# Kernel tuning notes

Hardware: AMD Instinct MI355X
Metric: run time of the kernel (lower is better)

The kernel has to match this reference:

```python
import jax, jax.numpy as jnp
import numpy as np

EPS = 1e-5
NUM_HEADS = 8
KEY_DEPTH = 128   # base_filters * key_expansion
VAL_DEPTH = 256   # base_filters * value_expansion
C_IN = 256


def conv1x1(x, w):
    # x: [N, Cin, L], w: [Cout, Cin] (1x1 conv, no bias)
    return jnp.einsum('oc,ncl->nol', w, x)


def group_norm1(x, w, b, eps=EPS):
    # torch GroupNorm(1, C) on [N, C, L]: normalize over (C, L) per sample,
    # per-channel affine.
    mu = jnp.mean(x, axis=(1, 2), keepdims=True)
    var = jnp.var(x, axis=(1, 2), keepdims=True)
    xn = (x - mu) * jax.lax.rsqrt(var + eps)
    return xn * w[None, :, None] + b[None, :, None]


def layer_norm_last2(x, eps=EPS):
    # freshly-constructed nn.LayerNorm([A, B]): weight=1, bias=0 -> pure norm
    mu = jnp.mean(x, axis=(-2, -1), keepdims=True)
    var = jnp.var(x, axis=(-2, -1), keepdims=True)
    return (x - mu) * jax.lax.rsqrt(var + eps)


def gelu(x):
    return jax.nn.gelu(x, approximate=False)  # torch F.gelu default (erf)


def setup_inputs() -> dict:
    key = jax.random.key(0)
    ks = jax.random.split(key, 16)
    N, L = 8, 1024
    qkv_out = 2 * KEY_DEPTH + VAL_DEPTH  # 512

    def w(k, shape, std=0.02):
        return jax.random.normal(k, shape, jnp.float32) * std

    def gw(k, c):
        return 1.0 + 0.1 * jax.random.normal(k, (c,), jnp.float32)

    return {
        'f': jax.random.normal(ks[0], (N, C_IN, L), jnp.float32),
        'w_z': w(ks[1], (C_IN, C_IN), np.sqrt(2.0 / C_IN)),
        'gz_w': gw(ks[2], C_IN), 'gz_b': w(ks[3], (C_IN,)),
        'w_qkv': w(ks[4], (qkv_out, C_IN), C_IN ** -0.5),
        'gq_w': gw(ks[5], qkv_out), 'gq_b': w(ks[6], (qkv_out,)),
        'w_out': w(ks[7], (C_IN, VAL_DEPTH), np.sqrt(2.0 / VAL_DEPTH)),
        'go_w': gw(ks[8], C_IN), 'go_b': w(ks[9], (C_IN,)),
        'w_ffn1': w(ks[10], (2 * C_IN, C_IN), np.sqrt(2.0 / C_IN)),
        'g1_w': gw(ks[11], 2 * C_IN), 'g1_b': w(ks[12], (2 * C_IN,)),
        'w_ffn2': w(ks[13], (C_IN, 2 * C_IN), np.sqrt(1.0 / C_IN)),
        'g2_w': gw(ks[14], C_IN), 'g2_b': w(ks[15], (C_IN,)),
    }


def reference(f, w_z, gz_w, gz_b, w_qkv, gq_w, gq_b, w_out, go_w, go_b,
              w_ffn1, g1_w, g1_b, w_ffn2, g2_w, g2_b):
    N, C, L = f.shape
    H = NUM_HEADS

    z = gelu(group_norm1(conv1x1(gelu(f), w_z), gz_w, gz_b))
    qkv = group_norm1(conv1x1(z, w_qkv), gq_w, gq_b)
    q, k, v = jnp.split(qkv, [KEY_DEPTH, 2 * KEY_DEPTH], axis=1)
    q = q.reshape(N, H, KEY_DEPTH // H, L)
    k = k.reshape(N, H, KEY_DEPTH // H, L)
    v = v.reshape(N, H, VAL_DEPTH // H, L)

    # [N, H, L, L] similarity, no scaling, then LayerNorm over full LxL map
    logits = jnp.einsum('nhcl,nhcm->nhlm', q, k)
    logits = layer_norm_last2(logits)

    # scatter-mask: diagonal -> -inf for every head
    eye = jnp.eye(L, dtype=bool)[None, None]  # [1,1,L,L]
    logits = jnp.where(eye, -jnp.inf, logits)

    attn = jax.nn.softmax(logits.astype(jnp.float32), axis=-1)
    attn = jnp.where(jnp.isnan(attn), 0.0, attn)

    out = jnp.einsum('nhlm,nhdm->nhdl', attn, v).reshape(N, VAL_DEPTH, L)
    out = gelu(layer_norm_last2(out))  # LayerNorm([C_v, L]), fresh params

    out = group_norm1(conv1x1(out, w_out), go_w, go_b)
    f = gelu(f + out)

    h = gelu(group_norm1(conv1x1(f, w_ffn1), g1_w, g1_b))
    h = group_norm1(conv1x1(h, w_ffn2), g2_w, g2_b)
    return gelu(f + h)
```

## Files before the change

### kernel.cpp

```cpp
#include <hip/hip_runtime.h>

#define LSEQ 1024

typedef __attribute__((ext_vector_type(8))) short bf16x8;
typedef __attribute__((ext_vector_type(4))) float f32x4;

__device__ __forceinline__ float gelu_f(float x){
    return 0.5f*x*(1.0f+erff(x*0.7071067811865476f));
}

__device__ __forceinline__ unsigned f2bf1(float x){
    unsigned u = __float_as_uint(x);
    return (u + 0x7fffu + ((u>>16)&1u)) >> 16;
}
__device__ __forceinline__ unsigned packbf(float lo, float hi){
    return f2bf1(lo) | (f2bf1(hi)<<16);
}

__global__ __launch_bounds__(256) void pack_weights(
    const float* __restrict__ w0, const float* __restrict__ w1,
    const float* __restrict__ w2, const float* __restrict__ w3,
    const float* __restrict__ w4, unsigned short* __restrict__ dst)
{
    int idx4 = blockIdx.x*256 + threadIdx.x;
    const float* src; int off4;
    if(idx4 < 16384){ src=w0; off4=idx4; }
    else if(idx4 < 49152){ src=w1; off4=idx4-16384; }
    else if(idx4 < 65536){ src=w2; off4=idx4-49152; }
    else if(idx4 < 98304){ src=w3; off4=idx4-65536; }
    else { src=w4; off4=idx4-98304; }
    float4 v = ((const float4*)src)[off4];
    uint2 p; p.x = packbf(v.x,v.y); p.y = packbf(v.z,v.w);
    ((uint2*)dst)[idx4] = p;
}

__global__ __launch_bounds__(256,2) void xform_bf16(
    const float* __restrict__ src, const float* __restrict__ res,
    const float* __restrict__ stats,
    const float* __restrict__ gw, const float* __restrict__ gb,
    float cnt_inv, int C, unsigned short* __restrict__ dst)
{
    __shared__ float T[64][68];
    int n = blockIdx.z;
    int ltile = blockIdx.x*64, ctile = blockIdx.y*64;
    int tid = threadIdx.x;

    float mu=0.f, istd=1.f;
    if(stats){
        float s1 = stats[2*n], s2 = stats[2*n+1];
        mu = s1*cnt_inv;
        istd = rsqrtf(s2*cnt_inv - mu*mu + 1e-5f);
    }
    const float* s = src + (size_t)n*C*LSEQ;
    const float* r = res ? res + (size_t)n*C*LSEQ : nullptr;

    int cl = tid>>4, l4 = (tid&15)*4;
    #pragma unroll
    for(int p=0;p<4;p++){
        int c_loc = p*16 + cl;
        int c = ctile + c_loc;
        float w_ = 1.f, b_ = 0.f;
        if(stats){ w_ = istd; b_ = -mu*istd; }
        if(gw){ b_ = gb[c] + b_*gw[c]; w_ *= gw[c]; }
        float4 v = *(const float4*)&s[(size_t)c*LSEQ + ltile + l4];
        float4 t;
        t.x = v.x*w_+b_; t.y = v.y*w_+b_; t.z = v.z*w_+b_; t.w = v.w*w_+b_;
        if(r){
            float4 rv = *(const float4*)&r[(size_t)c*LSEQ + ltile + l4];
            t.x += rv.x; t.y += rv.y; t.z += rv.z; t.w += rv.w;
        }
        t.x = gelu_f(t.x); t.y = gelu_f(t.y); t.z = gelu_f(t.z); t.w = gelu_f(t.w);
        *(float4*)&T[c_loc][l4] = t;
    }
    __syncthreads();

    int l_loc = tid>>2, cg = (tid&3)*16;
    uint4 o0, o1;
    o0.x = packbf(T[cg+0][l_loc],  T[cg+1][l_loc]);
    o0.y = packbf(T[cg+2][l_loc],  T[cg+3][l_loc]);
    o0.z = packbf(T[cg+4][l_loc],  T[cg+5][l_loc]);
    o0.w = packbf(T[cg+6][l_loc],  T[cg+7][l_loc]);
    o1.x = packbf(T[cg+8][l_loc],  T[cg+9][l_loc]);
    o1.y = packbf(T[cg+10][l_loc], T[cg+11][l_loc]);
    o1.z = packbf(T[cg+12][l_loc], T[cg+13][l_loc]);
    o1.w = packbf(T[cg+14][l_loc], T[cg+15][l_loc]);
    unsigned short* d = dst + (size_t)n*LSEQ*C + (size_t)(ltile+l_loc)*C + ctile + cg;
    *(uint4*)d = o0;
    *(uint4*)(d+8) = o1;
}

__global__ __launch_bounds__(256,2) void gemm_bf16(
    const unsigned short* __restrict__ Abf,
    const unsigned short* __restrict__ Bbf,
    float* __restrict__ C,
    int M, int K,
    float* __restrict__ out_stats)
{
    __shared__ short As[64*40];
    __shared__ short Bs[64*40];

    int tid = threadIdx.x;
    int n = blockIdx.z, n0 = blockIdx.x*64, m0 = blockIdx.y*64;
    int wave = tid>>6, lane = tid&63;
    int col = lane&15, quad = lane>>4;
    int sr = tid>>2, sk = (tid&3)*8;

    const unsigned short* apt = Abf + (size_t)(m0+sr)*K + sk;
    const unsigned short* bpt = Bbf + ((size_t)n*LSEQ + n0+sr)*K + sk;

    f32x4 acc[4];
    #pragma unroll
    for(int t=0;t<4;t++) acc[t] = (f32x4){0.f,0.f,0.f,0.f};

    uint4 a = *(const uint4*)apt;
    uint4 b = *(const uint4*)bpt;

    for(int k0=0; k0<K; k0+=32){
        __syncthreads();
        *(uint4*)&As[sr*40 + sk] = a;
        *(uint4*)&Bs[sr*40 + sk] = b;
        __syncthreads();
        if(k0+32 < K){
            a = *(const uint4*)(apt + k0+32);
            b = *(const uint4*)(bpt + k0+32);
        }
        bf16x8 af = *(bf16x8*)&As[(wave*16+col)*40 + quad*8];
        #pragma unroll
        for(int t=0;t<4;t++){
            bf16x8 bf = *(bf16x8*)&Bs[(t*16+col)*40 + quad*8];
            acc[t] = __builtin_amdgcn_mfma_f32_16x16x32_bf16(af, bf, acc[t], 0,0,0);
        }
    }

    __syncthreads();
    size_t cbase = (size_t)n*M*LSEQ;
    float lsum=0.f, lsq=0.f;
    #pragma unroll
    for(int t=0;t<4;t++){
        #pragma unroll
        for(int r2=0;r2<4;r2++){
            int m = m0 + wave*16 + quad*4 + r2;
            int l = n0 + t*16 + col;
            float v = acc[t][r2];
            C[cbase + (size_t)m*LSEQ + l] = v;
            lsum += v; lsq += v*v;
        }
    }
    float* scr = (float*)As;
    scr[tid] = lsum; scr[256+tid] = lsq;
    __syncthreads();
    for(int s=128;s>0;s>>=1){
        if(tid<s){ scr[tid]+=scr[tid+s]; scr[256+tid]+=scr[256+tid+s]; }
        __syncthreads();
    }
    if(tid==0){
        atomicAdd(&out_stats[2*n],   scr[0]);
        atomicAdd(&out_stats[2*n+1], scr[256]);
    }
}

__global__ __launch_bounds__(256,2) void head_cov(
    const float* __restrict__ qkv,
    const float* __restrict__ s_qkv,
    const float* __restrict__ gq_w, const float* __restrict__ gq_b,
    float* __restrict__ covq, float* __restrict__ covk,
    float* __restrict__ sumq, float* __restrict__ sumk)
{
    __shared__ float Kq[16*132];
    __shared__ float Kk[16*132];
    int b = blockIdx.x;
    int head = b>>3, chunk = b&7;
    int n = head>>3, h = head&7;
    int tid = threadIdx.x;
    int m0 = chunk*128;

    float s1 = s_qkv[2*n], s2v = s_qkv[2*n+1];
    float mu  = s1*(1.f/524288.f);
    float var = s2v*(1.f/524288.f) - mu*mu;
    float istd = rsqrtf(var + 1e-5f);

    const float* base = qkv + (size_t)n*512*LSEQ;
    int m = tid&127, cg = tid>>7;
    #pragma unroll
    for(int cc=0;cc<8;cc++){
        int c = cg*8+cc;
        int chq = h*16+c, chk = 128+h*16+c;
        Kq[c*132+m] = (base[(size_t)chq*LSEQ+m0+m]-mu)*istd*gq_w[chq]+gq_b[chq];
        Kk[c*132+m] = (base[(size_t)chk*LSEQ+m0+m]-mu)*istd*gq_w[chk]+gq_b[chk];
    }
    __syncthreads();

    int i = tid>>4, j = tid&15;
    float q0=0,q1=0,q2=0,q3=0, k0=0,k1=0,k2=0,k3=0;
    for(int mm=0;mm<128;mm+=4){
        float4 qa = *(const float4*)&Kq[i*132+mm];
        float4 qb = *(const float4*)&Kq[j*132+mm];
        q0 += qa.x*qb.x; q1 += qa.y*qb.y; q2 += qa.z*qb.z; q3 += qa.w*qb.w;
        float4 ka = *(const float4*)&Kk[i*132+mm];
        float4 kb = *(const float4*)&Kk[j*132+mm];
        k0 += ka.x*kb.x; k1 += ka.y*kb.y; k2 += ka.z*kb.z; k3 += ka.w*kb.w;
    }
    atomicAdd(&covq[head*256 + i*16 + j], (q0+q1)+(q2+q3));
    atomicAdd(&covk[head*256 + i*16 + j], (k0+k1)+(k2+k3));

    if(i==0){
        float s=0.f;
        for(int mm=0;mm<128;mm+=4){
            float4 v = *(const float4*)&Kq[j*132+mm];
            s += (v.x+v.y)+(v.z+v.w);
        }
        atomicAdd(&sumq[head*16+j], s);
    }
    if(i==1){
        float s=0.f;
        for(int mm=0;mm<128;mm+=4){
            float4 v = *(const float4*)&Kk[j*132+mm];
            s += (v.x+v.y)+(v.z+v.w);
        }
        atomicAdd(&sumk[head*16+j], s);
    }
}

__global__ __launch_bounds__(256) void head_fin(
    const float* __restrict__ covq, const float* __restrict__ covk,
    const float* __restrict__ sumq, const float* __restrict__ sumk,
    float* __restrict__ istd_head)
{
    int tid = threadIdx.x;
    int head = tid>>2, part = tid&3;
    double S2 = 0.0;
    #pragma unroll 8
    for(int e=part*64; e<part*64+64; e++)
        S2 += (double)covq[head*256+e]*(double)covk[head*256+e];
    S2 += __shfl_xor(S2,1);
    S2 += __shfl_xor(S2,2);
    if(part==0){
        double S1 = 0.0;
        for(int c=0;c<16;c++) S1 += (double)sumq[head*16+c]*(double)sumk[head*16+c];
        double cnt = 1048576.0;
        double mean = S1/cnt;
        double v2 = S2/cnt - mean*mean;
        if(v2 < 0.0) v2 = 0.0;
        istd_head[head] = (float)(1.0/sqrt(v2 + 1e-5));
    }
}

__global__ __launch_bounds__(256) void attn_kernel(
    const float* __restrict__ qkv,
    const float* __restrict__ s_qkv,
    const float* __restrict__ gq_w, const float* __restrict__ gq_b,
    const float* __restrict__ istd_head,
    float* __restrict__ out,
    float* __restrict__ out_stats)
{
    __shared__ short Qs[128*40];
    __shared__ short Ks[128*40];
    __shared__ short Vs[32*136];
    __shared__ short Ps[128*152];
    __shared__ float bounds_l[128];
    __shared__ float issum_l[128];
    __shared__ float sred4[4];

    int b = blockIdx.x;
    int head = b&63, rb = b>>6;
    int n = head>>3, h = head&7;
    int tid = threadIdx.x;
    int wv = tid>>6, lane = tid&63;
    int col = lane&15, quad = lane>>4;
    int l0 = rb*128;

    const float* base = qkv + (size_t)n*512*LSEQ;
    float s1 = s_qkv[2*n], s2v = s_qkv[2*n+1];
    float mu  = s1*(1.f/524288.f);
    float var = s2v*(1.f/524288.f) - mu*mu;
    float istd = rsqrtf(var + 1e-5f);
    float ih = istd_head[head];

    {
        int row = tid>>1, hf = tid&1;
        uint4 z = {0,0,0,0};
        *(uint4*)&Qs[row*40 + 16 + hf*8] = z;
        *(uint4*)&Ks[row*40 + 16 + hf*8] = z;
    }

    {
        int row = tid>>1, cg = tid&1;
        float qn2p = 0.f;
        float qv[8];
        #pragma unroll
        for(int cc=0;cc<8;cc++){
            int ch = h*16 + cg*8 + cc;
            float w_ = gq_w[ch]*istd, b_ = gq_b[ch]-mu*istd*gq_w[ch];
            float x = base[(size_t)ch*LSEQ + l0 + row];
            float v = x*w_ + b_;
            qv[cc] = v;
            qn2p += v*v;
        }
        uint4 pq;
        pq.x = packbf(qv[0],qv[1]); pq.y = packbf(qv[2],qv[3]);
        pq.z = packbf(qv[4],qv[5]); pq.w = packbf(qv[6],qv[7]);
        *(uint4*)&Qs[row*40 + cg*8] = pq;
        float oth = __shfl_xor(qn2p, 1);
        if(cg==0) bounds_l[row] = sqrtf(qn2p + oth);
    }

    {
        float kn2max = 0.f;
        #pragma unroll
        for(int j=0;j<4;j++){
            int m = tid + j*256;
            float s = 0.f;
            for(int c=0;c<16;c++){
                int ch = 128+h*16+c;
                float x = base[(size_t)ch*LSEQ + m];
                float kv = (x-mu)*istd*gq_w[ch]+gq_b[ch];
                s += kv*kv;
            }
            kn2max = fmaxf(kn2max, s);
        }
        #pragma unroll
        for(int d=1;d<64;d<<=1) kn2max = fmaxf(kn2max, __shfl_xor(kn2max,d));
        if(lane==0) sred4[wv] = kn2max;
    }
    __syncthreads();
    float kmax = sqrtf(fmaxf(fmaxf(sred4[0],sred4[1]),fmaxf(sred4[2],sred4[3])));

    bf16x8 qf[2];
    float B2[2]; int grow[2];
    #pragma unroll
    for(int t=0;t<2;t++){
        int rl = (2*wv+t)*16 + col;
        qf[t] = *(bf16x8*)&Qs[rl*40 + quad*8];
        B2[t] = bounds_l[rl]*kmax*ih;
        grow[t] = l0 + rl;
    }

    int km_l = tid>>1, kg = tid&1;
    float kw8[8], kb8[8];
    #pragma unroll
    for(int cc=0;cc<8;cc++){
        int ch = 128+h*16+kg*8+cc;
        kw8[cc] = gq_w[ch]*istd;
        kb8[cc] = gq_b[ch]-mu*istd*gq_w[ch];
    }
    int vd = tid>>3, vmg = tid&7;
    float vw, vb;
    {
        int ch = 256+h*32+vd;
        vw = gq_w[ch]*istd;
        vb = gq_b[ch]-mu*istd*gq_w[ch];
    }
    const float* kp = base + (size_t)(128+h*16+kg*8)*LSEQ + km_l;
    const float* vp = base + (size_t)(256+h*32+vd)*LSEQ + vmg*16;

    f32x4 acc[2][2];
    #pragma unroll
    for(int t=0;t<2;t++){ acc[t][0]=(f32x4){0,0,0,0}; acc[t][1]=(f32x4){0,0,0,0}; }
    float ssum[2] = {0.f,0.f};
    const f32x4 zero4 = {0.f,0.f,0.f,0.f};

    for(int mc=0;mc<8;mc++){
        int M0 = mc*128;
        {
            float kv[8];
            #pragma unroll
            for(int cc=0;cc<8;cc++)
                kv[cc] = kp[(size_t)cc*LSEQ + M0]*kw8[cc] + kb8[cc];
            uint4 pk;
            pk.x=packbf(kv[0],kv[1]); pk.y=packbf(kv[2],kv[3]);
            pk.z=packbf(kv[4],kv[5]); pk.w=packbf(kv[6],kv[7]);
            *(uint4*)&Ks[km_l*40 + kg*8] = pk;
        }
        {
            float4 x0 = *(const float4*)&vp[M0];
            float4 x1 = *(const float4*)&vp[M0+4];
            float4 x2 = *(const float4*)&vp[M0+8];
            float4 x3 = *(const float4*)&vp[M0+12];
            uint4 p0, p1;
            p0.x = packbf(x0.x*vw+vb, x0.y*vw+vb);
            p0.y = packbf(x0.z*vw+vb, x0.w*vw+vb);
            p0.z = packbf(x1.x*vw+vb, x1.y*vw+vb);
            p0.w = packbf(x1.z*vw+vb, x1.w*vw+vb);
            p1.x = packbf(x2.x*vw+vb, x2.y*vw+vb);
            p1.y = packbf(x2.z*vw+vb, x2.w*vw+vb);
            p1.z = packbf(x3.x*vw+vb, x3.y*vw+vb);
            p1.w = packbf(x3.z*vw+vb, x3.w*vw+vb);
            *(uint4*)&Vs[vd*136 + vmg*16]     = p0;
            *(uint4*)&Vs[vd*136 + vmg*16 + 8] = p1;
        }
        __syncthreads();

        #pragma unroll
        for(int mt=0;mt<8;mt++){
            bf16x8 ak = *(bf16x8*)&Ks[(mt*16+col)*40 + quad*8];
            #pragma unroll
            for(int t=0;t<2;t++){
                f32x4 sc = __builtin_amdgcn_mfma_f32_16x16x32_bf16(ak, qf[t], zero4, 0,0,0);
                int mbase = M0 + mt*16 + quad*4;
                float pr[4];
                #pragma unroll
                for(int r=0;r<4;r++){
                    float e = __expf(fmaf(sc[r], ih, -B2[t]));
                    pr[r] = (mbase + r == grow[t]) ? 0.f : e;
                    ssum[t] += pr[r];
                }
                uint2 pw;
                pw.x = packbf(pr[0],pr[1]); pw.y = packbf(pr[2],pr[3]);
                *(uint2*)&Ps[((2*wv+t)*16+col)*152 + mt*16 + quad*4] = pw;
            }
        }
        #pragma unroll
        for(int kk=0;kk<4;kk++){
            bf16x8 bv0 = *(bf16x8*)&Vs[( col)*136 + kk*32 + quad*8];
            bf16x8 bv1 = *(bf16x8*)&Vs[((16+col))*136 + kk*32 + quad*8];
            #pragma unroll
            for(int t=0;t<2;t++){
                bf16x8 ap = *(bf16x8*)&Ps[((2*wv+t)*16+col)*152 + kk*32 + quad*8];
                acc[t][0] = __builtin_amdgcn_mfma_f32_16x16x32_bf16(ap, bv0, acc[t][0], 0,0,0);
                acc[t][1] = __builtin_amdgcn_mfma_f32_16x16x32_bf16(ap, bv1, acc[t][1], 0,0,0);
            }
        }
        __syncthreads();
    }

    #pragma unroll
    for(int t=0;t<2;t++){
        float v = ssum[t];
        v += __shfl_xor(v,16);
        v += __shfl_xor(v,32);
        if(quad==0) issum_l[(2*wv+t)*16+col] = v;
    }
    __syncthreads();
    if(tid<128) issum_l[tid] = 1.f/issum_l[tid];
    __syncthreads();

    float* ep = (float*)Ps;
    #pragma unroll
    for(int t=0;t<2;t++)
        #pragma unroll
        for(int dt=0;dt<2;dt++)
            *(f32x4*)&ep[(dt*16+col)*132 + (2*wv+t)*16 + quad*4] = acc[t][dt];
    __syncthreads();

    float lsum=0.f, lsq=0.f;
    size_t obase = (size_t)n*262144 + (size_t)h*32*LSEQ + l0;
    #pragma unroll
    for(int t=0;t<16;t++){
        int idx = t*256 + tid;
        int d = idx>>7, row = idx&127;
        float y = ep[d*132+row]*issum_l[row];
        out[obase + (size_t)d*LSEQ + row] = y;
        lsum += y; lsq += y*y;
    }
    float* red = (float*)Ks;
    red[tid]=lsum; red[256+tid]=lsq;
    __syncthreads();
    for(int s=128;s>0;s>>=1){
        if(tid<s){ red[tid]+=red[tid+s]; red[256+tid]+=red[256+tid+s]; }
        __syncthreads();
    }
    if(tid==0){
        atomicAdd(&out_stats[2*n],   red[0]);
        atomicAdd(&out_stats[2*n+1], red[256]);
    }
}

__global__ __launch_bounds__(256) void ew_final(
    const float* __restrict__ f, const float* __restrict__ x,
    const float* __restrict__ h2,
    const float* __restrict__ sx, const float* __restrict__ sh,
    const float* __restrict__ go_w, const float* __restrict__ go_b,
    const float* __restrict__ g2_w, const float* __restrict__ g2_b,
    float* __restrict__ out)
{
    int idx = blockIdx.x*256 + threadIdx.x;
    int n = idx >> 16;
    int c = (idx >> 8) & 255;
    float mux, isx, muh, ish;
    {
        float s1 = sx[2*n], s2 = sx[2*n+1];
        mux = s1*(1.f/262144.f);
        isx = rsqrtf(s2*(1.f/262144.f) - mux*mux + 1e-5f);
        float t1 = sh[2*n], t2 = sh[2*n+1];
        muh = t1*(1.f/262144.f);
        ish = rsqrtf(t2*(1.f/262144.f) - muh*muh + 1e-5f);
    }
    float wo = go_w[c]*isx, bo = go_b[c]-mux*isx*go_w[c];
    float w2 = g2_w[c]*ish, b2 = g2_b[c]-muh*ish*g2_w[c];
    float4 xv = ((const float4*)x)[idx];
    float4 fv = ((const float4*)f)[idx];
    float4 hv = ((const float4*)h2)[idx];
    float4 ov;
    float f1;
    f1 = gelu_f(fv.x + xv.x*wo+bo); ov.x = gelu_f(f1 + hv.x*w2+b2);
    f1 = gelu_f(fv.y + xv.y*wo+bo); ov.y = gelu_f(f1 + hv.y*w2+b2);
    f1 = gelu_f(fv.z + xv.z*wo+bo); ov.z = gelu_f(f1 + hv.z*w2+b2);
    f1 = gelu_f(fv.w + xv.w*wo+bo); ov.w = gelu_f(f1 + hv.w*w2+b2);
    ((float4*)out)[idx] = ov;
}

extern "C" void kernel_launch(void* const* d_in, const int* in_sizes, int n_in,
                              void* d_out, int out_size, void* d_ws, size_t ws_size,
                              hipStream_t stream) {
    const float* f     = (const float*)d_in[0];
    const float* w_z   = (const float*)d_in[1];
    const float* gz_w  = (const float*)d_in[2];
    const float* gz_b  = (const float*)d_in[3];
    const float* w_qkv = (const float*)d_in[4];
    const float* gq_w  = (const float*)d_in[5];
    const float* gq_b  = (const float*)d_in[6];
    const float* w_out = (const float*)d_in[7];
    const float* go_w  = (const float*)d_in[8];
    const float* go_b  = (const float*)d_in[9];
    const float* w_f1  = (const float*)d_in[10];
    const float* g1_w  = (const float*)d_in[11];
    const float* g1_b  = (const float*)d_in[12];
    const float* w_f2  = (const float*)d_in[13];
    const float* g2_w  = (const float*)d_in[14];
    const float* g2_b  = (const float*)d_in[15];

    float* ws = (float*)d_ws;
    float* stats = ws;
    float* s_z    = stats + 0;
    float* s_qkv  = stats + 16;
    float* s_attn = stats + 32;
    float* s_x    = stats + 48;
    float* s_h1   = stats + 64;
    float* s_h2   = stats + 80;
    float* istdh  = stats + 96;

    float* qkvF = ws + 256;
    float* z0F  = qkvF + 4194304;
    float* xF   = z0F + 2097152;
    unsigned short* t0 = (unsigned short*)(xF + 2097152);
    unsigned short* t1 = t0 + 2097152;
    unsigned short* wp = t1 + 2097152;
    unsigned short* t4 = (unsigned short*)z0F;
    unsigned short* wp_z   = wp;
    unsigned short* wp_qkv = wp + 65536;
    unsigned short* wp_out = wp + 196608;
    unsigned short* wp_f1  = wp + 262144;
    unsigned short* wp_f2  = wp + 393216;

    float* covq = xF;
    float* covk = xF + 16384;
    float* sumq = xF + 32768;
    float* sumk = xF + 33792;

    float* outp = (float*)d_out;

    hipMemsetAsync(stats, 0, 256*sizeof(float), stream);
    hipMemsetAsync(covq, 0, 34816*sizeof(float), stream);

    dim3 blk(256);
    pack_weights<<<512,blk,0,stream>>>(w_z, w_qkv, w_out, w_f1, w_f2, wp);
    xform_bf16<<<dim3(16,4,8),blk,0,stream>>>(f, nullptr, nullptr, nullptr, nullptr,
        0.f, 256, t0);
    gemm_bf16<<<dim3(16,4,8),blk,0,stream>>>(wp_z, t0, z0F, 256, 256, s_z);
    xform_bf16<<<dim3(16,4,8),blk,0,stream>>>(z0F, nullptr, s_z, gz_w, gz_b,
        1.f/262144.f, 256, t1);
    gemm_bf16<<<dim3(16,8,8),blk,0,stream>>>(wp_qkv, t1, qkvF, 512, 256, s_qkv);
    head_cov<<<512,blk,0,stream>>>(qkvF, s_qkv, gq_w, gq_b, covq, covk, sumq, sumk);
    head_fin<<<1,blk,0,stream>>>(covq, covk, sumq, sumk, istdh);
    attn_kernel<<<512,blk,0,stream>>>(qkvF, s_qkv, gq_w, gq_b, istdh, z0F, s_attn);
    xform_bf16<<<dim3(16,4,8),blk,0,stream>>>(z0F, nullptr, s_attn, nullptr, nullptr,
        1.f/262144.f, 256, t0);
    gemm_bf16<<<dim3(16,4,8),blk,0,stream>>>(wp_out, t0, xF, 256, 256, s_x);
    xform_bf16<<<dim3(16,4,8),blk,0,stream>>>(xF, f, s_x, go_w, go_b,
        1.f/262144.f, 256, t1);
    gemm_bf16<<<dim3(16,8,8),blk,0,stream>>>(wp_f1, t1, qkvF, 512, 256, s_h1);
    xform_bf16<<<dim3(16,8,8),blk,0,stream>>>(qkvF, nullptr, s_h1, g1_w, g1_b,
        1.f/524288.f, 512, t4);
    gemm_bf16<<<dim3(16,4,8),blk,0,stream>>>(wp_f2, t4, qkvF, 256, 512, s_h2);
    ew_final<<<2048,blk,0,stream>>>(f, xF, qkvF, s_x, s_h2,
        go_w, go_b, g2_w, g2_b, outp);
}
```

Baseline: 320.3 us.

## Halve attention row tile to double blocks; stage full K panel in GEMM

The attention kernel now processes 64 query rows per block instead of 128, with one 16-row tile per wave, and the launch grid doubles to 1024 blocks. The aim is more parallelism and lower per-block register and LDS use, at the cost of every block re-staging and re-scanning the head's full K and V. Separately, the GEMM loads a whole 256-wide K panel into LDS in one step instead of 32-wide slices. That cuts barrier count but drops the register prefetch overlap and raises LDS use per block.

```diff
diff --git a/kernel.cpp b/kernel.cpp
--- a/kernel.cpp
+++ b/kernel.cpp
@@ -96,39 +96,43 @@
     int M, int K,
     float* __restrict__ out_stats)
 {
-    __shared__ short As[64*40];
-    __shared__ short Bs[64*40];
+    __shared__ short As[64*264];
+    __shared__ short Bs[64*264];
 
     int tid = threadIdx.x;
     int n = blockIdx.z, n0 = blockIdx.x*64, m0 = blockIdx.y*64;
     int wave = tid>>6, lane = tid&63;
     int col = lane&15, quad = lane>>4;
-    int sr = tid>>2, sk = (tid&3)*8;
-
-    const unsigned short* apt = Abf + (size_t)(m0+sr)*K + sk;
-    const unsigned short* bpt = Bbf + ((size_t)n*LSEQ + n0+sr)*K + sk;
+    int srow = tid>>2, sks = (tid&3)*8;
+
+    const unsigned short* apt = Abf + (size_t)(m0+srow)*K + sks;
+    const unsigned short* bpt = Bbf + ((size_t)n*LSEQ + n0+srow)*K + sks;
 
     f32x4 acc[4];
     #pragma unroll
     for(int t=0;t<4;t++) acc[t] = (f32x4){0.f,0.f,0.f,0.f};
 
-    uint4 a = *(const uint4*)apt;
-    uint4 b = *(const uint4*)bpt;
-
-    for(int k0=0; k0<K; k0+=32){
+    for(int kp=0; kp<K; kp+=256){
         __syncthreads();
-        *(uint4*)&As[sr*40 + sk] = a;
-        *(uint4*)&Bs[sr*40 + sk] = b;
+        uint4 av[8], bw[8];
+        #pragma unroll
+        for(int i=0;i<8;i++) av[i] = *(const uint4*)(apt + kp + i*32);
+        #pragma unroll
+        for(int i=0;i<8;i++) bw[i] = *(const uint4*)(bpt + kp + i*32);
+        #pragma unroll
+        for(int i=0;i<8;i++) *(uint4*)&As[srow*264 + sks + i*32] = av[i];
+        #pragma unroll
+        for(int i=0;i<8;i++) *(uint4*)&Bs[srow*264 + sks + i*32] = bw[i];
         __syncthreads();
-        if(k0+32 < K){
-            a = *(const uint4*)(apt + k0+32);
-            b = *(const uint4*)(bpt + k0+32);
-        }
-        bf16x8 af = *(bf16x8*)&As[(wave*16+col)*40 + quad*8];
-        #pragma unroll
-        for(int t=0;t<4;t++){
-            bf16x8 bf = *(bf16x8*)&Bs[(t*16+col)*40 + quad*8];
-            acc[t] = __builtin_amdgcn_mfma_f32_16x16x32_bf16(af, bf, acc[t], 0,0,0);
+
+        #pragma unroll
+        for(int kc=0;kc<8;kc++){
+            bf16x8 af = *(bf16x8*)&As[(wave*16+col)*264 + kc*32 + quad*8];
+            #pragma unroll
+            for(int t=0;t<4;t++){
+                bf16x8 bf = *(bf16x8*)&Bs[(t*16+col)*264 + kc*32 + quad*8];
+                acc[t] = __builtin_amdgcn_mfma_f32_16x16x32_bf16(af, bf, acc[t], 0,0,0);
+            }
         }
     }
 
@@ -253,12 +257,12 @@
     float* __restrict__ out,
     float* __restrict__ out_stats)
 {
-    __shared__ short Qs[128*40];
+    __shared__ short Qs[64*40];
     __shared__ short Ks[128*40];
     __shared__ short Vs[32*136];
-    __shared__ short Ps[128*152];
-    __shared__ float bounds_l[128];
-    __shared__ float issum_l[128];
+    __shared__ short Ps[64*152];
+    __shared__ float bounds_l[64];
+    __shared__ float issum_l[64];
     __shared__ float sred4[4];
 
     int b = blockIdx.x;
@@ -267,7 +271,7 @@
     int tid = threadIdx.x;
     int wv = tid>>6, lane = tid&63;
     int col = lane&15, quad = lane>>4;
-    int l0 = rb*128;
+    int l0 = rb*64;
 
     const float* base = qkv + (size_t)n*512*LSEQ;
     float s1 = s_qkv[2*n], s2v = s_qkv[2*n+1];
@@ -277,31 +281,34 @@
     float ih = istd_head[head];
 
     {
+        uint4 z = {0,0,0,0};
+        if(tid < 128){
+            int row = tid>>1, hf = tid&1;
+            *(uint4*)&Qs[row*40 + 16 + hf*8] = z;
+        }
         int row = tid>>1, hf = tid&1;
-        uint4 z = {0,0,0,0};
-        *(uint4*)&Qs[row*40 + 16 + hf*8] = z;
         *(uint4*)&Ks[row*40 + 16 + hf*8] = z;
     }
 
     {
-        int row = tid>>1, cg = tid&1;
+        int row = tid>>2, cg = tid&3;
         float qn2p = 0.f;
-        float qv[8];
-        #pragma unroll
-        for(int cc=0;cc<8;cc++){
-            int ch = h*16 + cg*8 + cc;
+        float qv[4];
+        #pragma unroll
+        for(int cc=0;cc<4;cc++){
+            int ch = h*16 + cg*4 + cc;
             float w_ = gq_w[ch]*istd, b_ = gq_b[ch]-mu*istd*gq_w[ch];
             float x = base[(size_t)ch*LSEQ + l0 + row];
             float v = x*w_ + b_;
             qv[cc] = v;
             qn2p += v*v;
         }
-        uint4 pq;
+        uint2 pq;
         pq.x = packbf(qv[0],qv[1]); pq.y = packbf(qv[2],qv[3]);
-        pq.z = packbf(qv[4],qv[5]); pq.w = packbf(qv[6],qv[7]);
-        *(uint4*)&Qs[row*40 + cg*8] = pq;
-        float oth = __shfl_xor(qn2p, 1);
-        if(cg==0) bounds_l[row] = sqrtf(qn2p + oth);
+        *(uint2*)&Qs[row*40 + cg*4] = pq;
+        qn2p += __shfl_xor(qn2p, 1);
+        qn2p += __shfl_xor(qn2p, 2);
+        if(cg==0) bounds_l[row] = sqrtf(qn2p);
     }
 
     {
@@ -325,15 +332,10 @@
     __syncthreads();
     float kmax = sqrtf(fmaxf(fmaxf(sred4[0],sred4[1]),fmaxf(sred4[2],sred4[3])));
 
-    bf16x8 qf[2];
-    float B2[2]; int grow[2];
-    #pragma unroll
-    for(int t=0;t<2;t++){
-        int rl = (2*wv+t)*16 + col;
-        qf[t] = *(bf16x8*)&Qs[rl*40 + quad*8];
-        B2[t] = bounds_l[rl]*kmax*ih;
-        grow[t] = l0 + rl;
-    }
+    int rl = wv*16 + col;
+    bf16x8 qf = *(bf16x8*)&Qs[rl*40 + quad*8];
+    float B2 = bounds_l[rl]*kmax*ih;
+    int grow = l0 + rl;
 
     int km_l = tid>>1, kg = tid&1;
     float kw8[8], kb8[8];
@@ -353,10 +355,9 @@
     const float* kp = base + (size_t)(128+h*16+kg*8)*LSEQ + km_l;
     const float* vp = base + (size_t)(256+h*32+vd)*LSEQ + vmg*16;
 
-    f32x4 acc[2][2];
-    #pragma unroll
-    for(int t=0;t<2;t++){ acc[t][0]=(f32x4){0,0,0,0}; acc[t][1]=(f32x4){0,0,0,0}; }
-    float ssum[2] = {0.f,0.f};
+    f32x4 acc[2];
+    acc[0]=(f32x4){0,0,0,0}; acc[1]=(f32x4){0,0,0,0};
+    float ssum = 0.f;
     const f32x4 zero4 = {0.f,0.f,0.f,0.f};
 
     for(int mc=0;mc<8;mc++){
@@ -393,62 +394,53 @@
         #pragma unroll
         for(int mt=0;mt<8;mt++){
             bf16x8 ak = *(bf16x8*)&Ks[(mt*16+col)*40 + quad*8];
+            f32x4 sc = __builtin_amdgcn_mfma_f32_16x16x32_bf16(ak, qf, zero4, 0,0,0);
+            int mbase = M0 + mt*16 + quad*4;
+            float pr[4];
             #pragma unroll
-            for(int t=0;t<2;t++){
-                f32x4 sc = __builtin_amdgcn_mfma_f32_16x16x32_bf16(ak, qf[t], zero4, 0,0,0);
-                int mbase = M0 + mt*16 + quad*4;
-                float pr[4];
-                #pragma unroll
-                for(int r=0;r<4;r++){
-                    float e = __expf(fmaf(sc[r], ih, -B2[t]));
-                    pr[r] = (mbase + r == grow[t]) ? 0.f : e;
-                    ssum[t] += pr[r];
-                }
-                uint2 pw;
-                pw.x = packbf(pr[0],pr[1]); pw.y = packbf(pr[2],pr[3]);
-                *(uint2*)&Ps[((2*wv+t)*16+col)*152 + mt*16 + quad*4] = pw;
+            for(int r=0;r<4;r++){
+                float e = __expf(fmaf(sc[r], ih, -B2));
+                pr[r] = (mbase + r == grow) ? 0.f : e;
+                ssum += pr[r];
             }
+            uint2 pw;
+            pw.x = packbf(pr[0],pr[1]); pw.y = packbf(pr[2],pr[3]);
+            *(uint2*)&Ps[rl*152 + mt*16 + quad*4] = pw;
         }
         #pragma unroll
         for(int kk=0;kk<4;kk++){
             bf16x8 bv0 = *(bf16x8*)&Vs[( col)*136 + kk*32 + quad*8];
-            bf16x8 bv1 = *(bf16x8*)&Vs[((16+col))*136 + kk*32 + quad*8];
-            #pragma unroll
-            for(int t=0;t<2;t++){
-                bf16x8 ap = *(bf16x8*)&Ps[((2*wv+t)*16+col)*152 + kk*32 + quad*8];
-                acc[t][0] = __builtin_amdgcn_mfma_f32_16x16x32_bf16(ap, bv0, acc[t][0], 0,0,0);
-                acc[t][1] = __builtin_amdgcn_mfma_f32_16x16x32_bf16(ap, bv1, acc[t][1], 0,0,0);
-            }
+            bf16x8 bv1 = *(bf16x8*)&Vs[(16+col)*136 + kk*32 + quad*8];
+            bf16x8 ap = *(bf16x8*)&Ps[rl*152 + kk*32 + quad*8];
+            acc[0] = __builtin_amdgcn_mfma_f32_16x16x32_bf16(ap, bv0, acc[0], 0,0,0);
+            acc[1] = __builtin_amdgcn_mfma_f32_16x16x32_bf16(ap, bv1, acc[1], 0,0,0);
         }
         __syncthreads();
     }
 
-    #pragma unroll
-    for(int t=0;t<2;t++){
-        float v = ssum[t];
+    {
+        float v = ssum;
         v += __shfl_xor(v,16);
         v += __shfl_xor(v,32);
-        if(quad==0) issum_l[(2*wv+t)*16+col] = v;
-    }
-    __syncthreads();
-    if(tid<128) issum_l[tid] = 1.f/issum_l[tid];
+        if(quad==0) issum_l[rl] = v;
+    }
+    __syncthreads();
+    if(tid<64) issum_l[tid] = 1.f/issum_l[tid];
     __syncthreads();
 
     float* ep = (float*)Ps;
     #pragma unroll
-    for(int t=0;t<2;t++)
-        #pragma unroll
-        for(int dt=0;dt<2;dt++)
-            *(f32x4*)&ep[(dt*16+col)*132 + (2*wv+t)*16 + quad*4] = acc[t][dt];
+    for(int dt=0;dt<2;dt++)
+        *(f32x4*)&ep[(dt*16+col)*68 + wv*16 + quad*4] = acc[dt];
     __syncthreads();
 
     float lsum=0.f, lsq=0.f;
     size_t obase = (size_t)n*262144 + (size_t)h*32*LSEQ + l0;
     #pragma unroll
-    for(int t=0;t<16;t++){
+    for(int t=0;t<8;t++){
         int idx = t*256 + tid;
-        int d = idx>>7, row = idx&127;
-        float y = ep[d*132+row]*issum_l[row];
+        int d = idx>>6, row = idx&63;
+        float y = ep[d*68+row]*issum_l[row];
         out[obase + (size_t)d*LSEQ + row] = y;
         lsum += y; lsq += y*y;
     }
@@ -562,7 +554,7 @@
     gemm_bf16<<<dim3(16,8,8),blk,0,stream>>>(wp_qkv, t1, qkvF, 512, 256, s_qkv);
     head_cov<<<512,blk,0,stream>>>(qkvF, s_qkv, gq_w, gq_b, covq, covk, sumq, sumk);
     head_fin<<<1,blk,0,stream>>>(covq, covk, sumq, sumk, istdh);
-    attn_kernel<<<512,blk,0,stream>>>(qkvF, s_qkv, gq_w, gq_b, istdh, z0F, s_attn);
+    attn_kernel<<<1024,blk,0,stream>>>(qkvF, s_qkv, gq_w, gq_b, istdh, z0F, s_attn);
     xform_bf16<<<dim3(16,4,8),blk,0,stream>>>(z0F, nullptr, s_attn, nullptr, nullptr,
         1.f/262144.f, 256, t0);
     gemm_bf16<<<dim3(16,4,8),blk,0,stream>>>(wp_out, t0, xF, 256, 256, s_x);
```

After: 331.1 us. 1.03x slower.

## Merge prologue kernels and memsets, fold head_fin into attention, stage full K in GEMM

Applied to the files above, without the earlier changes.

Combines the two memsets, the weight packing and the first gelu/bf16 transpose into a single prologue launch, and computes the per-head LayerNorm inverse std inside each attention block so the single-block head_fin launch goes away. The GEMM now stages a 256-wide K slab of A and B in shared memory per sync instead of 32-wide chunks, which cuts barriers and lets the loads issue together. This raises shared memory use per block (about 67KB), which may lower occupancy, and every attention block now repeats the small per-head reduction.

```diff
diff --git a/kernel.cpp b/kernel.cpp
--- a/kernel.cpp
+++ b/kernel.cpp
@@ -17,21 +17,60 @@
     return f2bf1(lo) | (f2bf1(hi)<<16);
 }
 
-__global__ __launch_bounds__(256) void pack_weights(
+__global__ __launch_bounds__(256,2) void prologue(
     const float* __restrict__ w0, const float* __restrict__ w1,
     const float* __restrict__ w2, const float* __restrict__ w3,
-    const float* __restrict__ w4, unsigned short* __restrict__ dst)
+    const float* __restrict__ w4, unsigned short* __restrict__ wdst,
+    const float* __restrict__ f, unsigned short* __restrict__ t0,
+    float* __restrict__ stats, float* __restrict__ covs)
 {
-    int idx4 = blockIdx.x*256 + threadIdx.x;
-    const float* src; int off4;
-    if(idx4 < 16384){ src=w0; off4=idx4; }
-    else if(idx4 < 49152){ src=w1; off4=idx4-16384; }
-    else if(idx4 < 65536){ src=w2; off4=idx4-49152; }
-    else if(idx4 < 98304){ src=w3; off4=idx4-65536; }
-    else { src=w4; off4=idx4-98304; }
-    float4 v = ((const float4*)src)[off4];
-    uint2 p; p.x = packbf(v.x,v.y); p.y = packbf(v.z,v.w);
-    ((uint2*)dst)[idx4] = p;
+    __shared__ float T[64][68];
+    int b = blockIdx.x;
+    int tid = threadIdx.x;
+
+    if(b < 512){
+        int ltile = (b&15)*64, ctile = ((b>>4)&3)*64, n = b>>6;
+        const float* s = f + (size_t)n*256*LSEQ;
+        int cl = tid>>4, l4 = (tid&15)*4;
+        #pragma unroll
+        for(int p=0;p<4;p++){
+            int c_loc = p*16 + cl;
+            float4 v = *(const float4*)&s[(size_t)(ctile+c_loc)*LSEQ + ltile + l4];
+            float4 t;
+            t.x = gelu_f(v.x); t.y = gelu_f(v.y); t.z = gelu_f(v.z); t.w = gelu_f(v.w);
+            *(float4*)&T[c_loc][l4] = t;
+        }
+        __syncthreads();
+        int l_loc = tid>>2, cg = (tid&3)*16;
+        uint4 o0, o1;
+        o0.x = packbf(T[cg+0][l_loc],  T[cg+1][l_loc]);
+        o0.y = packbf(T[cg+2][l_loc],  T[cg+3][l_loc]);
+        o0.z = packbf(T[cg+4][l_loc],  T[cg+5][l_loc]);
+        o0.w = packbf(T[cg+6][l_loc],  T[cg+7][l_loc]);
+        o1.x = packbf(T[cg+8][l_loc],  T[cg+9][l_loc]);
+        o1.y = packbf(T[cg+10][l_loc], T[cg+11][l_loc]);
+        o1.z = packbf(T[cg+12][l_loc], T[cg+13][l_loc]);
+        o1.w = packbf(T[cg+14][l_loc], T[cg+15][l_loc]);
+        unsigned short* d = t0 + (size_t)n*LSEQ*256 + (size_t)(ltile+l_loc)*256 + ctile + cg;
+        *(uint4*)d = o0;
+        *(uint4*)(d+8) = o1;
+    } else if(b < 1024){
+        int idx4 = (b-512)*256 + tid;
+        const float* src; int off4;
+        if(idx4 < 16384){ src=w0; off4=idx4; }
+        else if(idx4 < 49152){ src=w1; off4=idx4-16384; }
+        else if(idx4 < 65536){ src=w2; off4=idx4-49152; }
+        else if(idx4 < 98304){ src=w3; off4=idx4-65536; }
+        else { src=w4; off4=idx4-98304; }
+        float4 v = ((const float4*)src)[off4];
+        uint2 p; p.x = packbf(v.x,v.y); p.y = packbf(v.z,v.w);
+        ((uint2*)wdst)[idx4] = p;
+    } else if(b == 1024){
+        if(tid < 64) ((float4*)stats)[tid] = (float4){0.f,0.f,0.f,0.f};
+    } else {
+        int i = (b-1025)*256 + tid;
+        ((float4*)covs)[i] = (float4){0.f,0.f,0.f,0.f};
+    }
 }
 
 __global__ __launch_bounds__(256,2) void xform_bf16(
@@ -96,39 +135,43 @@
     int M, int K,
     float* __restrict__ out_stats)
 {
-    __shared__ short As[64*40];
-    __shared__ short Bs[64*40];
+    __shared__ short As[64*264];
+    __shared__ short Bs[64*264];
 
     int tid = threadIdx.x;
     int n = blockIdx.z, n0 = blockIdx.x*64, m0 = blockIdx.y*64;
     int wave = tid>>6, lane = tid&63;
     int col = lane&15, quad = lane>>4;
-    int sr = tid>>2, sk = (tid&3)*8;
-
-    const unsigned short* apt = Abf + (size_t)(m0+sr)*K + sk;
-    const unsigned short* bpt = Bbf + ((size_t)n*LSEQ + n0+sr)*K + sk;
+    int srow = tid>>2, sks = (tid&3)*8;
+
+    const unsigned short* apt = Abf + (size_t)(m0+srow)*K + sks;
+    const unsigned short* bpt = Bbf + ((size_t)n*LSEQ + n0+srow)*K + sks;
 
     f32x4 acc[4];
     #pragma unroll
     for(int t=0;t<4;t++) acc[t] = (f32x4){0.f,0.f,0.f,0.f};
 
-    uint4 a = *(const uint4*)apt;
-    uint4 b = *(const uint4*)bpt;
-
-    for(int k0=0; k0<K; k0+=32){
-        __syncthreads();
-        *(uint4*)&As[sr*40 + sk] = a;
-        *(uint4*)&Bs[sr*40 + sk] = b;
-        __syncthreads();
-        if(k0+32 < K){
-            a = *(const uint4*)(apt + k0+32);
-            b = *(const uint4*)(bpt + k0+32);
-        }
-        bf16x8 af = *(bf16x8*)&As[(wave*16+col)*40 + quad*8];
-        #pragma unroll
-        for(int t=0;t<4;t++){
-            bf16x8 bf = *(bf16x8*)&Bs[(t*16+col)*40 + quad*8];
-            acc[t] = __builtin_amdgcn_mfma_f32_16x16x32_bf16(af, bf, acc[t], 0,0,0);
+    for(int kp=0; kp<K; kp+=256){
+        __syncthreads();
+        uint4 av[8], bw[8];
+        #pragma unroll
+        for(int i=0;i<8;i++) av[i] = *(const uint4*)(apt + kp + i*32);
+        #pragma unroll
+        for(int i=0;i<8;i++) bw[i] = *(const uint4*)(bpt + kp + i*32);
+        #pragma unroll
+        for(int i=0;i<8;i++) *(uint4*)&As[srow*264 + sks + i*32] = av[i];
+        #pragma unroll
+        for(int i=0;i<8;i++) *(uint4*)&Bs[srow*264 + sks + i*32] = bw[i];
+        __syncthreads();
+
+        #pragma unroll
+        for(int kc=0;kc<8;kc++){
+            bf16x8 af = *(bf16x8*)&As[(wave*16+col)*264 + kc*32 + quad*8];
+            #pragma unroll
+            for(int t=0;t<4;t++){
+                bf16x8 bf = *(bf16x8*)&Bs[(t*16+col)*264 + kc*32 + quad*8];
+                acc[t] = __builtin_amdgcn_mfma_f32_16x16x32_bf16(af, bf, acc[t], 0,0,0);
+            }
         }
     }
 
@@ -221,35 +264,12 @@
     }
 }
 
-__global__ __launch_bounds__(256) void head_fin(
-    const float* __restrict__ covq, const float* __restrict__ covk,
-    const float* __restrict__ sumq, const float* __restrict__ sumk,
-    float* __restrict__ istd_head)
-{
-    int tid = threadIdx.x;
-    int head = tid>>2, part = tid&3;
-    double S2 = 0.0;
-    #pragma unroll 8
-    for(int e=part*64; e<part*64+64; e++)
-        S2 += (double)covq[head*256+e]*(double)covk[head*256+e];
-    S2 += __shfl_xor(S2,1);
-    S2 += __shfl_xor(S2,2);
-    if(part==0){
-        double S1 = 0.0;
-        for(int c=0;c<16;c++) S1 += (double)sumq[head*16+c]*(double)sumk[head*16+c];
-        double cnt = 1048576.0;
-        double mean = S1/cnt;
-        double v2 = S2/cnt - mean*mean;
-        if(v2 < 0.0) v2 = 0.0;
-        istd_head[head] = (float)(1.0/sqrt(v2 + 1e-5));
-    }
-}
-
 __global__ __launch_bounds__(256) void attn_kernel(
     const float* __restrict__ qkv,
     const float* __restrict__ s_qkv,
     const float* __restrict__ gq_w, const float* __restrict__ gq_b,
-    const float* __restrict__ istd_head,
+    const float* __restrict__ covq, const float* __restrict__ covk,
+    const float* __restrict__ sumq, const float* __restrict__ sumk,
     float* __restrict__ out,
     float* __restrict__ out_stats)
 {
@@ -269,12 +289,36 @@
     int col = lane&15, quad = lane>>4;
     int l0 = rb*128;
 
+    float ih;
+    {
+        float* fs = (float*)Ps;
+        fs[tid] = covq[head*256+tid]*covk[head*256+tid];
+        __syncthreads();
+        for(int s=128;s>0;s>>=1){
+            if(tid<s) fs[tid]+=fs[tid+s];
+            __syncthreads();
+        }
+        if(tid==0){
+            double S2 = (double)fs[0];
+            double S1 = 0.0;
+            for(int c=0;c<16;c++)
+                S1 += (double)sumq[head*16+c]*(double)sumk[head*16+c];
+            double cnt = 1048576.0;
+            double mean = S1/cnt;
+            double v2 = S2/cnt - mean*mean;
+            if(v2 < 0.0) v2 = 0.0;
+            fs[0] = (float)(1.0/sqrt(v2 + 1e-5));
+        }
+        __syncthreads();
+        ih = fs[0];
+        __syncthreads();
+    }
+
     const float* base = qkv + (size_t)n*512*LSEQ;
     float s1 = s_qkv[2*n], s2v = s_qkv[2*n+1];
     float mu  = s1*(1.f/524288.f);
     float var = s2v*(1.f/524288.f) - mu*mu;
     float istd = rsqrtf(var + 1e-5f);
-    float ih = istd_head[head];
 
     {
         int row = tid>>1, hf = tid&1;
@@ -527,7 +571,6 @@
     float* s_x    = stats + 48;
     float* s_h1   = stats + 64;
     float* s_h2   = stats + 80;
-    float* istdh  = stats + 96;
 
     float* qkvF = ws + 256;
     float* z0F  = qkvF + 4194304;
@@ -549,20 +592,16 @@
 
     float* outp = (float*)d_out;
 
-    hipMemsetAsync(stats, 0, 256*sizeof(float), stream);
-    hipMemsetAsync(covq, 0, 34816*sizeof(float), stream);
-
     dim3 blk(256);
-    pack_weights<<<512,blk,0,stream>>>(w_z, w_qkv, w_out, w_f1, w_f2, wp);
-    xform_bf16<<<dim3(16,4,8),blk,0,stream>>>(f, nullptr, nullptr, nullptr, nullptr,
-        0.f, 256, t0);
+    prologue<<<1059,blk,0,stream>>>(w_z, w_qkv, w_out, w_f1, w_f2, wp,
+        f, t0, stats, covq);
     gemm_bf16<<<dim3(16,4,8),blk,0,stream>>>(wp_z, t0, z0F, 256, 256, s_z);
     xform_bf16<<<dim3(16,4,8),blk,0,stream>>>(z0F, nullptr, s_z, gz_w, gz_b,
         1.f/262144.f, 256, t1);
     gemm_bf16<<<dim3(16,8,8),blk,0,stream>>>(wp_qkv, t1, qkvF, 512, 256, s_qkv);
     head_cov<<<512,blk,0,stream>>>(qkvF, s_qkv, gq_w, gq_b, covq, covk, sumq, sumk);
-    head_fin<<<1,blk,0,stream>>>(covq, covk, sumq, sumk, istdh);
-    attn_kernel<<<512,blk,0,stream>>>(qkvF, s_qkv, gq_w, gq_b, istdh, z0F, s_attn);
+    attn_kernel<<<512,blk,0,stream>>>(qkvF, s_qkv, gq_w, gq_b,
+        covq, covk, sumq, sumk, z0F, s_attn);
     xform_bf16<<<dim3(16,4,8),blk,0,stream>>>(z0F, nullptr, s_attn, nullptr, nullptr,
         1.f/262144.f, 256, t0);
     gemm_bf16<<<dim3(16,4,8),blk,0,stream>>>(wp_out, t0, xF, 256, 256, s_x);
```

New measurement: 300.1 us. 6.3% less time.
